# Kernel optimization log

Measured on AMD Instinct MI355X. Metric: run time of the kernel, lower is better.

Reference implementation:

```python
import jax, jax.numpy as jnp
import numpy as np

# Static problem dims (all graphs equal-sized so adaptive pool = uniform bins)
B = 64          # graphs
N = 2048        # nodes per graph
E = 16          # node_emb_dim
H_OUT, W_OUT = 32, 4   # AdaptiveAvgPool2d output -> pooled_dim = 128
COND = 64       # cond_emb_dim
HID = 512       # mlp_h_dim
BN_EPS = 1e-5


def _lin_init(key, out_d, in_d):
    kw, kb = jax.random.split(key)
    lim = 1.0 / np.sqrt(in_d)
    W = jax.random.uniform(kw, (out_d, in_d), jnp.float32, -lim, lim)
    b = jax.random.uniform(kb, (out_d,), jnp.float32, -lim, lim)
    return W, b


def setup_inputs() -> dict:
    key = jax.random.key(0)
    ks = jax.random.split(key, 6)
    Ntot = B * N
    x = jax.random.normal(ks[0], (Ntot, E), jnp.float32)
    batch = jnp.repeat(jnp.arange(B, dtype=jnp.int32), N)  # sorted segment ids
    cond = jax.random.normal(ks[1], (Ntot, COND), jnp.float32)
    mlp_in = COND + H_OUT * W_OUT  # 192
    W1, b1 = _lin_init(ks[2], HID, mlp_in)
    W2, b2 = _lin_init(ks[3], HID, HID)
    W3, b3 = _lin_init(ks[4], 3, HID)
    g1 = jnp.ones((HID,), jnp.float32); be1 = jnp.zeros((HID,), jnp.float32)
    g2 = jnp.ones((HID,), jnp.float32); be2 = jnp.zeros((HID,), jnp.float32)
    return {"x": x, "batch": batch, "conditioner_z_ref": cond,
            "W1": W1, "b1": b1, "g1": g1, "be1": be1,
            "W2": W2, "b2": b2, "g2": g2, "be2": be2,
            "W3": W3, "b3": b3}


def _bn_gelu(h, g, be):
    # BatchNorm1d in training mode: biased batch stats over the node axis
    m = h.mean(axis=0)
    v = h.var(axis=0)
    h = g * (h - m) * jax.lax.rsqrt(v + BN_EPS) + be
    return jax.nn.gelu(h, approximate=False)


def reference(x, batch, conditioner_z_ref, W1, b1, g1, be1, W2, b2, g2, be2, W3, b3):
    # Per-graph adaptive avg pool: since N % H_OUT == 0 and E % W_OUT == 0,
    # AdaptiveAvgPool2d is exactly mean over uniform (N/H_OUT, E/W_OUT) bins.
    xb = x.reshape(B, H_OUT, N // H_OUT, W_OUT, E // W_OUT)
    batch_pooled = xb.mean(axis=(2, 4)).reshape(B, H_OUT * W_OUT)  # [B, 128]
    pooled_per_node = batch_pooled[batch]                           # gather to [Ntot, 128]
    h = jnp.concatenate([conditioner_z_ref, pooled_per_node], axis=1)  # [Ntot, 192]
    h = _bn_gelu(h @ W1.T + b1, g1, be1)
    h = _bn_gelu(h @ W2.T + b2, g2, be2)
    return h @ W3.T + b3  # [Ntot, 3] predicted coords
```

## Files before the change

kernel.cpp:

```cpp
#include <hip/hip_runtime.h>
#include <hip/hip_bf16.h>
#include <math.h>
#include <stdint.h>

#define B_GRAPHS 64
#define N_NODES  2048
#define E_DIM    16
#define M_TOT    (B_GRAPHS * N_NODES)
#define K_COND   64
#define MLP_IN   192
#define HID      512
#define POOLD    128
#define BN_EPS   1e-5f

typedef __attribute__((ext_vector_type(8))) short bfrag8;
typedef __attribute__((ext_vector_type(4))) float facc4;

__device__ __forceinline__ unsigned short f2b(float f) {
    unsigned int x = __builtin_bit_cast(unsigned int, f);
    unsigned int r = x + 0x7fffu + ((x >> 16) & 1u);
    return (unsigned short)(r >> 16);
}
__device__ __forceinline__ float b2f(unsigned short u) {
    unsigned int x = ((unsigned int)u) << 16;
    return __builtin_bit_cast(float, x);
}

__device__ __forceinline__ float gelu_fast(float y) {
    float x  = y * 0.70710678118654752440f;
    float ax = fabsf(x);
    float t  = __builtin_amdgcn_rcpf(fmaf(0.3275911f, ax, 1.0f));
    float p  = fmaf(1.061405429f, t, -1.453152027f);
    p = fmaf(p, t, 1.421413741f);
    p = fmaf(p, t, -0.284496736f);
    p = fmaf(p, t, 0.254829592f);
    p = p * t;
    float e = __expf(-x * x);
    float erfax = fmaf(-p, e, 1.0f);
    float erfx  = copysignf(erfax, x);
    return 0.5f * y * (1.0f + erfx);
}

#define GLOAD_LDS16(g, l)                                                        \
    __builtin_amdgcn_global_load_lds(                                            \
        (const __attribute__((address_space(1))) unsigned int*)(const void*)(g), \
        (__attribute__((address_space(3))) unsigned int*)(void*)(l), 16, 0, 0)

__global__ void pool_kernel(const float* __restrict__ x, float* __restrict__ pooled) {
    int g = blockIdx.x;
    int t = threadIdx.x;
    int h = t >> 2, w = t & 3;
    const float* base = x + (size_t)g * N_NODES * E_DIM + (size_t)h * 64 * E_DIM + w * 4;
    float s = 0.f;
    #pragma unroll 4
    for (int r = 0; r < 64; ++r) {
        float4 v = *reinterpret_cast<const float4*>(base + (size_t)r * E_DIM);
        s += v.x + v.y + v.z + v.w;
    }
    pooled[g * POOLD + h * 4 + w] = s * (1.0f / 256.0f);
}

__global__ void gbias_kernel(const float* __restrict__ pooled, const float* __restrict__ W1,
                             const float* __restrict__ b1, float* __restrict__ gbias) {
    int g = blockIdx.x;
    int n = threadIdx.x;
    const float* pr = pooled + g * POOLD;
    const float* wr = W1 + (size_t)n * MLP_IN + K_COND;
    float s = b1[n];
    #pragma unroll 4
    for (int k = 0; k < POOLD; ++k) s = fmaf(pr[k], wr[k], s);
    gbias[g * HID + n] = s;
}

__global__ __launch_bounds__(256) void cvt_kernel(const float* __restrict__ s,
                                                  unsigned short* __restrict__ d) {
    size_t i = ((size_t)blockIdx.x * 256 + threadIdx.x) * 8;
    float4 v0 = *reinterpret_cast<const float4*>(s + i);
    float4 v1 = *reinterpret_cast<const float4*>(s + i + 4);
    unsigned short t[8] = {f2b(v0.x), f2b(v0.y), f2b(v0.z), f2b(v0.w),
                           f2b(v1.x), f2b(v1.y), f2b(v1.z), f2b(v1.w)};
    *reinterpret_cast<bfrag8*>(d + i) = *reinterpret_cast<bfrag8*>(t);
}

__device__ __forceinline__ bfrag8 load_f32x8_as_bf16(const float* p) {
    float4 v0 = *reinterpret_cast<const float4*>(p);
    float4 v1 = *reinterpret_cast<const float4*>(p + 4);
    unsigned short t[8] = {f2b(v0.x), f2b(v0.y), f2b(v0.z), f2b(v0.w),
                           f2b(v1.x), f2b(v1.y), f2b(v1.z), f2b(v1.w)};
    return *reinterpret_cast<bfrag8*>(t);
}

__global__ __launch_bounds__(256) void gemm1_kernel(const float* __restrict__ A,
                                                    const float* __restrict__ W,
                                                    const int* __restrict__ batch,
                                                    const float* __restrict__ gbias,
                                                    float* __restrict__ sums,
                                                    unsigned short* __restrict__ C) {
    __shared__ float sArr[128], qArr[128];
    const int t = threadIdx.x;
    const int r0 = blockIdx.x * 128, c0 = blockIdx.y * 128;
    const int l = t & 63, w = t >> 6;
    const int wr = w >> 1, wc = w & 1;
    const int ln = l & 15, kg = l >> 4;
    if (t < 128) { sArr[t] = 0.f; qArr[t] = 0.f; }
    __syncthreads();

    facc4 acc[4][4];
    const facc4 z = {0.f, 0.f, 0.f, 0.f};
    #pragma unroll
    for (int a = 0; a < 4; ++a)
        #pragma unroll
        for (int b = 0; b < 4; ++b) acc[a][b] = z;

    #pragma unroll
    for (int ks = 0; ks < 2; ++ks) {
        bfrag8 af[4], bf[4];
        #pragma unroll
        for (int a = 0; a < 4; ++a)
            af[a] = load_f32x8_as_bf16(A + (size_t)(r0 + wr * 64 + a * 16 + ln) * K_COND + ks * 32 + kg * 8);
        #pragma unroll
        for (int b = 0; b < 4; ++b)
            bf[b] = load_f32x8_as_bf16(W + (size_t)(c0 + wc * 64 + b * 16 + ln) * MLP_IN + ks * 32 + kg * 8);
        #pragma unroll
        for (int a = 0; a < 4; ++a)
            #pragma unroll
            for (int b = 0; b < 4; ++b)
                acc[a][b] = __builtin_amdgcn_mfma_f32_16x16x32_bf16(af[a], bf[b], acc[a][b], 0, 0, 0);
    }

    float cs[4] = {0.f, 0.f, 0.f, 0.f}, cq[4] = {0.f, 0.f, 0.f, 0.f};
    #pragma unroll
    for (int a = 0; a < 4; ++a) {
        #pragma unroll
        for (int i = 0; i < 4; ++i) {
            int row = r0 + wr * 64 + a * 16 + kg * 4 + i;
            const float* gb = gbias + (size_t)batch[row] * HID;
            size_t rbase = (size_t)row * HID + c0 + wc * 64 + ln;
            #pragma unroll
            for (int b = 0; b < 4; ++b) {
                float v = acc[a][b][i] + gb[c0 + wc * 64 + b * 16 + ln];
                C[rbase + b * 16] = f2b(v);
                cs[b] += v; cq[b] = fmaf(v, v, cq[b]);
            }
        }
    }
    #pragma unroll
    for (int b = 0; b < 4; ++b) {
        cs[b] += __shfl_xor(cs[b], 16, 64); cq[b] += __shfl_xor(cq[b], 16, 64);
        cs[b] += __shfl_xor(cs[b], 32, 64); cq[b] += __shfl_xor(cq[b], 32, 64);
    }
    if (kg == 0) {
        #pragma unroll
        for (int b = 0; b < 4; ++b) {
            int cl = wc * 64 + b * 16 + ln;
            atomicAdd(&sArr[cl], cs[b]); atomicAdd(&qArr[cl], cq[b]);
        }
    }
    __syncthreads();
    if (t < 128) {
        atomicAdd(&sums[c0 + t], sArr[t]);
        atomicAdd(&sums[HID + c0 + t], qArr[t]);
    }
}

__global__ __launch_bounds__(512) void gemm2_kernel(const unsigned short* __restrict__ A,
                                                    const unsigned short* __restrict__ Bm,
                                                    const float* __restrict__ ssg,
                                                    const float* __restrict__ bias,
                                                    float* __restrict__ sums,
                                                    unsigned short* __restrict__ C) {
    __shared__ unsigned short As[128 * 32];
    __shared__ unsigned short Bs[256 * 32];
    __shared__ float lss[2 * HID];
    __shared__ float sArr[256], qArr[256];
    const int t = threadIdx.x;
    const int r0 = blockIdx.x * 128, c0 = blockIdx.y * 256;
    const int l = t & 63, w = t >> 6;
    const int wr = w >> 2, wc = w & 3;
    const int ln = l & 15, kg = l >> 4;
    const int arow = t >> 2, aslot = t & 3;

    lss[t] = ssg[t];
    lss[t + 512] = ssg[t + 512];
    if (t < 256) { sArr[t] = 0.f; qArr[t] = 0.f; }
    __syncthreads();

    facc4 acc[4][4];
    const facc4 z = {0.f, 0.f, 0.f, 0.f};
    #pragma unroll
    for (int a = 0; a < 4; ++a)
        #pragma unroll
        for (int b = 0; b < 4; ++b) acc[a][b] = z;

    const unsigned short* aptr = A + (size_t)(r0 + arow) * HID + aslot * 8;
    for (int kk = 0; kk < HID; kk += 32) {
        bfrag8 va = *reinterpret_cast<const bfrag8*>(aptr + kk);
        unsigned short tmp[8];
        #pragma unroll
        for (int j = 0; j < 8; ++j) {
            int col = kk + aslot * 8 + j;
            float xv = b2f((unsigned short)va[j]);
            float y = fmaf(xv, lss[col], lss[HID + col]);
            tmp[j] = f2b(gelu_fast(y));
        }
        *reinterpret_cast<bfrag8*>(&As[arow * 32 + aslot * 8]) = *reinterpret_cast<bfrag8*>(tmp);
        #pragma unroll
        for (int c = 0; c < 2; ++c) {
            int chunk = w * 2 + c;
            const unsigned short* gb =
                Bm + (size_t)(c0 + chunk * 16 + (l >> 2)) * HID + kk + (l & 3) * 8;
            GLOAD_LDS16(gb, &Bs[chunk * 512]);
        }
        __syncthreads();
        bfrag8 af[4], bf[4];
        #pragma unroll
        for (int a = 0; a < 4; ++a)
            af[a] = *reinterpret_cast<const bfrag8*>(&As[(wr * 64 + a * 16 + ln) * 32 + kg * 8]);
        #pragma unroll
        for (int b = 0; b < 4; ++b)
            bf[b] = *reinterpret_cast<const bfrag8*>(&Bs[(wc * 64 + b * 16 + ln) * 32 + kg * 8]);
        #pragma unroll
        for (int a = 0; a < 4; ++a)
            #pragma unroll
            for (int b = 0; b < 4; ++b)
                acc[a][b] = __builtin_amdgcn_mfma_f32_16x16x32_bf16(af[a], bf[b], acc[a][b], 0, 0, 0);
        __syncthreads();
    }

    float bb[4];
    #pragma unroll
    for (int b = 0; b < 4; ++b) bb[b] = bias[c0 + wc * 64 + b * 16 + ln];
    float cs[4] = {0.f, 0.f, 0.f, 0.f}, cq[4] = {0.f, 0.f, 0.f, 0.f};
    #pragma unroll
    for (int a = 0; a < 4; ++a) {
        #pragma unroll
        for (int i = 0; i < 4; ++i) {
            size_t rbase = (size_t)(r0 + wr * 64 + a * 16 + kg * 4 + i) * HID + c0 + wc * 64 + ln;
            #pragma unroll
            for (int b = 0; b < 4; ++b) {
                float v = acc[a][b][i] + bb[b];
                C[rbase + b * 16] = f2b(v);
                cs[b] += v; cq[b] = fmaf(v, v, cq[b]);
            }
        }
    }
    #pragma unroll
    for (int b = 0; b < 4; ++b) {
        cs[b] += __shfl_xor(cs[b], 16, 64); cq[b] += __shfl_xor(cq[b], 16, 64);
        cs[b] += __shfl_xor(cs[b], 32, 64); cq[b] += __shfl_xor(cq[b], 32, 64);
    }
    if (kg == 0) {
        #pragma unroll
        for (int b = 0; b < 4; ++b) {
            int cl = wc * 64 + b * 16 + ln;
            atomicAdd(&sArr[cl], cs[b]); atomicAdd(&qArr[cl], cq[b]);
        }
    }
    __syncthreads();
    if (t < 256) {
        atomicAdd(&sums[c0 + t], sArr[t]);
        atomicAdd(&sums[HID + c0 + t], qArr[t]);
    }
}

__global__ void finalize_kernel(const float* __restrict__ sums, const float* __restrict__ g,
                                const float* __restrict__ be, float* __restrict__ ss) {
    int n = threadIdx.x;
    float mean = sums[n] * (1.0f / M_TOT);
    float var = sums[HID + n] * (1.0f / M_TOT) - mean * mean;
    float sc = g[n] * rsqrtf(var + BN_EPS);
    ss[n] = sc;
    ss[HID + n] = be[n] - mean * sc;
}

__global__ __launch_bounds__(256) void g3_kernel(const unsigned short* __restrict__ H2,
                                                 const float* __restrict__ ss2,
                                                 const float* __restrict__ W3,
                                                 const float* __restrict__ b3,
                                                 float* __restrict__ out) {
    int t = threadIdx.x;
    int l = t & 63, w = t >> 6;
    int rsub = l >> 3, lk = l & 7;
    int row = blockIdx.x * 32 + w * 8 + rsub;
    const unsigned short* p = H2 + (size_t)row * HID;
    float o0 = 0.f, o1 = 0.f, o2 = 0.f;
    #pragma unroll
    for (int it = 0; it < 8; ++it) {
        int k = it * 64 + lk * 8;
        bfrag8 v = *reinterpret_cast<const bfrag8*>(p + k);
        #pragma unroll
        for (int j = 0; j < 8; ++j) {
            float x = b2f((unsigned short)v[j]);
            float y = fmaf(x, ss2[k + j], ss2[HID + k + j]);
            y = gelu_fast(y);
            o0 = fmaf(y, W3[k + j], o0);
            o1 = fmaf(y, W3[HID + k + j], o1);
            o2 = fmaf(y, W3[2 * HID + k + j], o2);
        }
    }
    #pragma unroll
    for (int m = 1; m < 8; m <<= 1) {
        o0 += __shfl_xor(o0, m, 64);
        o1 += __shfl_xor(o1, m, 64);
        o2 += __shfl_xor(o2, m, 64);
    }
    if (lk == 0) {
        out[(size_t)row * 3 + 0] = o0 + b3[0];
        out[(size_t)row * 3 + 1] = o1 + b3[1];
        out[(size_t)row * 3 + 2] = o2 + b3[2];
    }
}

extern "C" void kernel_launch(void* const* d_in, const int* in_sizes, int n_in,
                              void* d_out, int out_size, void* d_ws, size_t ws_size,
                              hipStream_t stream) {
    const float* x     = (const float*)d_in[0];
    const int*   batch = (const int*)d_in[1];
    const float* cond  = (const float*)d_in[2];
    const float* W1    = (const float*)d_in[3];
    const float* b1    = (const float*)d_in[4];
    const float* g1    = (const float*)d_in[5];
    const float* be1   = (const float*)d_in[6];
    const float* W2    = (const float*)d_in[7];
    const float* b2    = (const float*)d_in[8];
    const float* g2    = (const float*)d_in[9];
    const float* be2   = (const float*)d_in[10];
    const float* W3    = (const float*)d_in[11];
    const float* b3    = (const float*)d_in[12];

    const size_t H_BYTES = (size_t)M_TOT * HID * 2;
    if (ws_size < 2 * H_BYTES) return;
    char* ws = (char*)d_ws;
    unsigned short* H1 = (unsigned short*)ws;
    unsigned short* H2 = (unsigned short*)(ws + H_BYTES);

    float* outf   = (float*)d_out;
    float* pooled = outf;
    float* gbias  = pooled + B_GRAPHS * POOLD;
    float* sums1  = gbias + B_GRAPHS * HID;
    float* sums2  = sums1 + 2 * HID;
    float* ss1    = sums2 + 2 * HID;
    unsigned short* W2bf = (unsigned short*)(ss1 + 2 * HID);
    float* ss2 = (float*)ws;

    hipMemsetAsync(sums1, 0, 2 * 2 * HID * sizeof(float), stream);

    pool_kernel<<<B_GRAPHS, 128, 0, stream>>>(x, pooled);
    gbias_kernel<<<B_GRAPHS, HID, 0, stream>>>(pooled, W1, b1, gbias);
    cvt_kernel<<<(HID * HID / 8) / 256, 256, 0, stream>>>(W2, W2bf);

    gemm1_kernel<<<dim3(M_TOT / 128, HID / 128), 256, 0, stream>>>(
        cond, W1, batch, gbias, sums1, H1);
    finalize_kernel<<<1, HID, 0, stream>>>(sums1, g1, be1, ss1);

    gemm2_kernel<<<dim3(M_TOT / 128, HID / 256), 512, 0, stream>>>(
        H1, W2bf, ss1, b2, sums2, H2);
    finalize_kernel<<<1, HID, 0, stream>>>(sums2, g2, be2, ss2);

    g3_kernel<<<M_TOT / 32, 256, 0, stream>>>(H2, ss2, W3, b3, outf);
}
```

Measured before the change: 349.7 us.

## Double-buffer gemm2 with swizzled LDS, fuse pool/gbias and BN1 finalize

Several changes land together. The pool and gbias kernels are merged into one prep kernel, and the first BN finalize is folded into the gemm2 prologue, which removes two launches. gemm2 now double-buffers the A and B LDS tiles so the next K-slice loads and GELU transforms overlap the MFMAs, and it XOR-swizzles the LDS layout to cut bank conflicts. g3 stages the BN scale/shift and W3 in shared memory. The cost is more LDS per gemm2 block, which may lower occupancy, and every gemm2 block recomputes the finalize.

```diff
diff --git a/kernel.cpp b/kernel.cpp
--- a/kernel.cpp
+++ b/kernel.cpp
@@ -46,30 +46,29 @@
         (const __attribute__((address_space(1))) unsigned int*)(const void*)(g), \
         (__attribute__((address_space(3))) unsigned int*)(void*)(l), 16, 0, 0)
 
-__global__ void pool_kernel(const float* __restrict__ x, float* __restrict__ pooled) {
-    int g = blockIdx.x;
-    int t = threadIdx.x;
-    int h = t >> 2, w = t & 3;
-    const float* base = x + (size_t)g * N_NODES * E_DIM + (size_t)h * 64 * E_DIM + w * 4;
-    float s = 0.f;
+__global__ __launch_bounds__(512) void prep_kernel(const float* __restrict__ x,
+                                                   const float* __restrict__ W1,
+                                                   const float* __restrict__ b1,
+                                                   float* __restrict__ gbias) {
+    __shared__ float pl[POOLD];
+    int g = blockIdx.x, t = threadIdx.x;
+    if (t < 128) {
+        int h = t >> 2, w = t & 3;
+        const float* base = x + (size_t)g * N_NODES * E_DIM + (size_t)h * 64 * E_DIM + w * 4;
+        float s = 0.f;
+        #pragma unroll 4
+        for (int r = 0; r < 64; ++r) {
+            float4 v = *reinterpret_cast<const float4*>(base + (size_t)r * E_DIM);
+            s += v.x + v.y + v.z + v.w;
+        }
+        pl[h * 4 + w] = s * (1.0f / 256.0f);
+    }
+    __syncthreads();
+    const float* wr_ = W1 + (size_t)t * MLP_IN + K_COND;
+    float s = b1[t];
     #pragma unroll 4
-    for (int r = 0; r < 64; ++r) {
-        float4 v = *reinterpret_cast<const float4*>(base + (size_t)r * E_DIM);
-        s += v.x + v.y + v.z + v.w;
-    }
-    pooled[g * POOLD + h * 4 + w] = s * (1.0f / 256.0f);
-}
-
-__global__ void gbias_kernel(const float* __restrict__ pooled, const float* __restrict__ W1,
-                             const float* __restrict__ b1, float* __restrict__ gbias) {
-    int g = blockIdx.x;
-    int n = threadIdx.x;
-    const float* pr = pooled + g * POOLD;
-    const float* wr = W1 + (size_t)n * MLP_IN + K_COND;
-    float s = b1[n];
-    #pragma unroll 4
-    for (int k = 0; k < POOLD; ++k) s = fmaf(pr[k], wr[k], s);
-    gbias[g * HID + n] = s;
+    for (int k = 0; k < POOLD; ++k) s = fmaf(pl[k], wr_[k], s);
+    gbias[g * HID + t] = s;
 }
 
 __global__ __launch_bounds__(256) void cvt_kernel(const float* __restrict__ s,
@@ -165,12 +164,14 @@
 
 __global__ __launch_bounds__(512) void gemm2_kernel(const unsigned short* __restrict__ A,
                                                     const unsigned short* __restrict__ Bm,
-                                                    const float* __restrict__ ssg,
+                                                    const float* __restrict__ sums1,
+                                                    const float* __restrict__ g1,
+                                                    const float* __restrict__ be1,
                                                     const float* __restrict__ bias,
                                                     float* __restrict__ sums,
                                                     unsigned short* __restrict__ C) {
-    __shared__ unsigned short As[128 * 32];
-    __shared__ unsigned short Bs[256 * 32];
+    __shared__ unsigned short As[2][128 * 32];
+    __shared__ unsigned short Bs[2][256 * 32];
     __shared__ float lss[2 * HID];
     __shared__ float sArr[256], qArr[256];
     const int t = threadIdx.x;
@@ -179,11 +180,17 @@
     const int wr = w >> 2, wc = w & 3;
     const int ln = l & 15, kg = l >> 4;
     const int arow = t >> 2, aslot = t & 3;
-
-    lss[t] = ssg[t];
-    lss[t + 512] = ssg[t + 512];
+    const int rr = l >> 2, sp = l & 3;
+    const int bss = sp ^ ((rr >> 1) & 3);
+
+    {
+        float mean = sums1[t] * (1.0f / M_TOT);
+        float var  = sums1[HID + t] * (1.0f / M_TOT) - mean * mean;
+        float sc   = g1[t] * rsqrtf(var + BN_EPS);
+        lss[t] = sc;
+        lss[HID + t] = be1[t] - mean * sc;
+    }
     if (t < 256) { sArr[t] = 0.f; qArr[t] = 0.f; }
-    __syncthreads();
 
     facc4 acc[4][4];
     const facc4 z = {0.f, 0.f, 0.f, 0.f};
@@ -193,37 +200,70 @@
         for (int b = 0; b < 4; ++b) acc[a][b] = z;
 
     const unsigned short* aptr = A + (size_t)(r0 + arow) * HID + aslot * 8;
-    for (int kk = 0; kk < HID; kk += 32) {
-        bfrag8 va = *reinterpret_cast<const bfrag8*>(aptr + kk);
+    const int awslot = aslot ^ ((arow >> 1) & 3);
+
+    __syncthreads();
+
+    {
+        bfrag8 va = *reinterpret_cast<const bfrag8*>(aptr);
         unsigned short tmp[8];
         #pragma unroll
         for (int j = 0; j < 8; ++j) {
-            int col = kk + aslot * 8 + j;
+            int col = aslot * 8 + j;
             float xv = b2f((unsigned short)va[j]);
-            float y = fmaf(xv, lss[col], lss[HID + col]);
-            tmp[j] = f2b(gelu_fast(y));
-        }
-        *reinterpret_cast<bfrag8*>(&As[arow * 32 + aslot * 8]) = *reinterpret_cast<bfrag8*>(tmp);
+            tmp[j] = f2b(gelu_fast(fmaf(xv, lss[col], lss[HID + col])));
+        }
+        *reinterpret_cast<bfrag8*>(&As[0][arow * 32 + awslot * 8]) = *reinterpret_cast<bfrag8*>(tmp);
         #pragma unroll
         for (int c = 0; c < 2; ++c) {
             int chunk = w * 2 + c;
-            const unsigned short* gb =
-                Bm + (size_t)(c0 + chunk * 16 + (l >> 2)) * HID + kk + (l & 3) * 8;
-            GLOAD_LDS16(gb, &Bs[chunk * 512]);
-        }
-        __syncthreads();
+            const unsigned short* gb = Bm + (size_t)(c0 + chunk * 16 + rr) * HID + bss * 8;
+            GLOAD_LDS16(gb, &Bs[0][chunk * 512]);
+        }
+    }
+    __syncthreads();
+
+    for (int step = 0; step < 16; ++step) {
+        const int cur = step & 1;
         bfrag8 af[4], bf[4];
         #pragma unroll
-        for (int a = 0; a < 4; ++a)
-            af[a] = *reinterpret_cast<const bfrag8*>(&As[(wr * 64 + a * 16 + ln) * 32 + kg * 8]);
-        #pragma unroll
-        for (int b = 0; b < 4; ++b)
-            bf[b] = *reinterpret_cast<const bfrag8*>(&Bs[(wc * 64 + b * 16 + ln) * 32 + kg * 8]);
+        for (int a = 0; a < 4; ++a) {
+            int RA = wr * 64 + a * 16 + ln;
+            af[a] = *reinterpret_cast<const bfrag8*>(&As[cur][RA * 32 + (kg ^ ((RA >> 1) & 3)) * 8]);
+        }
+        #pragma unroll
+        for (int b = 0; b < 4; ++b) {
+            int RB = wc * 64 + b * 16 + ln;
+            bf[b] = *reinterpret_cast<const bfrag8*>(&Bs[cur][RB * 32 + (kg ^ ((RB >> 1) & 3)) * 8]);
+        }
+        bfrag8 va;
+        const bool pf = step < 15;
+        if (pf) {
+            const int kk = step * 32 + 32;
+            va = *reinterpret_cast<const bfrag8*>(aptr + kk);
+            #pragma unroll
+            for (int c = 0; c < 2; ++c) {
+                int chunk = w * 2 + c;
+                const unsigned short* gb = Bm + (size_t)(c0 + chunk * 16 + rr) * HID + kk + bss * 8;
+                GLOAD_LDS16(gb, &Bs[cur ^ 1][chunk * 512]);
+            }
+        }
         #pragma unroll
         for (int a = 0; a < 4; ++a)
             #pragma unroll
             for (int b = 0; b < 4; ++b)
                 acc[a][b] = __builtin_amdgcn_mfma_f32_16x16x32_bf16(af[a], bf[b], acc[a][b], 0, 0, 0);
+        if (pf) {
+            const int kk = step * 32 + 32;
+            unsigned short tmp[8];
+            #pragma unroll
+            for (int j = 0; j < 8; ++j) {
+                int col = kk + aslot * 8 + j;
+                float xv = b2f((unsigned short)va[j]);
+                tmp[j] = f2b(gelu_fast(fmaf(xv, lss[col], lss[HID + col])));
+            }
+            *reinterpret_cast<bfrag8*>(&As[cur ^ 1][arow * 32 + awslot * 8]) = *reinterpret_cast<bfrag8*>(tmp);
+        }
         __syncthreads();
     }
 
@@ -278,7 +318,12 @@
                                                  const float* __restrict__ W3,
                                                  const float* __restrict__ b3,
                                                  float* __restrict__ out) {
+    __shared__ float lss[2 * HID];
+    __shared__ float lw3[3 * HID];
     int t = threadIdx.x;
+    for (int i = t; i < 2 * HID; i += 256) lss[i] = ss2[i];
+    for (int i = t; i < 3 * HID; i += 256) lw3[i] = W3[i];
+    __syncthreads();
     int l = t & 63, w = t >> 6;
     int rsub = l >> 3, lk = l & 7;
     int row = blockIdx.x * 32 + w * 8 + rsub;
@@ -291,11 +336,11 @@
         #pragma unroll
         for (int j = 0; j < 8; ++j) {
             float x = b2f((unsigned short)v[j]);
-            float y = fmaf(x, ss2[k + j], ss2[HID + k + j]);
+            float y = fmaf(x, lss[k + j], lss[HID + k + j]);
             y = gelu_fast(y);
-            o0 = fmaf(y, W3[k + j], o0);
-            o1 = fmaf(y, W3[HID + k + j], o1);
-            o2 = fmaf(y, W3[2 * HID + k + j], o2);
+            o0 = fmaf(y, lw3[k + j], o0);
+            o1 = fmaf(y, lw3[HID + k + j], o1);
+            o2 = fmaf(y, lw3[2 * HID + k + j], o2);
         }
     }
     #pragma unroll
@@ -335,26 +380,23 @@
     unsigned short* H2 = (unsigned short*)(ws + H_BYTES);
 
     float* outf   = (float*)d_out;
-    float* pooled = outf;
-    float* gbias  = pooled + B_GRAPHS * POOLD;
+    float* gbias  = outf;
     float* sums1  = gbias + B_GRAPHS * HID;
     float* sums2  = sums1 + 2 * HID;
-    float* ss1    = sums2 + 2 * HID;
-    unsigned short* W2bf = (unsigned short*)(ss1 + 2 * HID);
+    unsigned short* W2bf = (unsigned short*)(sums2 + 2 * HID);
     float* ss2 = (float*)ws;
 
     hipMemsetAsync(sums1, 0, 2 * 2 * HID * sizeof(float), stream);
 
-    pool_kernel<<<B_GRAPHS, 128, 0, stream>>>(x, pooled);
-    gbias_kernel<<<B_GRAPHS, HID, 0, stream>>>(pooled, W1, b1, gbias);
+    prep_kernel<<<B_GRAPHS, 512, 0, stream>>>(x, W1, b1, gbias);
     cvt_kernel<<<(HID * HID / 8) / 256, 256, 0, stream>>>(W2, W2bf);
 
     gemm1_kernel<<<dim3(M_TOT / 128, HID / 128), 256, 0, stream>>>(
         cond, W1, batch, gbias, sums1, H1);
-    finalize_kernel<<<1, HID, 0, stream>>>(sums1, g1, be1, ss1);
 
     gemm2_kernel<<<dim3(M_TOT / 128, HID / 256), 512, 0, stream>>>(
-        H1, W2bf, ss1, b2, sums2, H2);
+        H1, W2bf, sums1, g1, be1, b2, sums2, H2);
+
     finalize_kernel<<<1, HID, 0, stream>>>(sums2, g2, be2, ss2);
 
     g3_kernel<<<M_TOT / 32, 256, 0, stream>>>(H2, ss2, W3, b3, outf);
```

New measurement: 335.4 us. -4.1%, faster.
